# Kernel optimization log

Measured on AMD Instinct MI355X. Metric: run time of the kernel, lower is better.

Reference implementation:

```python
import jax, jax.numpy as jnp
import numpy as np

MSFA = 4
EPS = 1e-6

def _mosaic_channel_index(H, W, m):
    # channel selected at pixel (h, w) is (h % m) * m + (w % m)
    h = jnp.arange(H) % m
    w = jnp.arange(W) % m
    return (h[:, None] * m + w[None, :]).astype(jnp.int32)  # [H, W]

def get_msfa(x, m):
    # x: [B, C, H, W] with C == m*m. Equivalent to the one-hot mask-multiply-sum:
    # a per-pixel gather of the channel dictated by the mosaic pattern.
    B, C, H, W = x.shape
    ch = _mosaic_channel_index(H, W, m)  # [H, W]
    idx = jnp.broadcast_to(ch[None, None], (B, 1, H, W))
    return jnp.take_along_axis(x, idx, axis=1)[:, 0]  # [B, H, W]

def charbonnier_mean(a, b):
    d = a - b
    return jnp.mean(jnp.sqrt(d * d + EPS))

def setup_inputs() -> dict:
    key = jax.random.key(0)
    k1, k2 = jax.random.split(key)
    B, C, H, W = 8, MSFA * MSFA, 512, 512
    X = jax.random.normal(k1, (B, C, H, W), dtype=jnp.float32)
    Y = jax.random.normal(k2, (B, C, H, W), dtype=jnp.float32)
    return {"X": X, "Y": Y}

def reference(X, Y):
    return charbonnier_mean(get_msfa(X, MSFA), get_msfa(Y, MSFA))
```

## Files before the change

kernel.cpp:

```cpp
#include <hip/hip_runtime.h>


#define EPS_F 1e-6f

constexpr int kBlocks  = 1024;
constexpr int kThreads = 256;
constexpr int kNPix    = 8 * 512 * 512;
constexpr int kPerThr  = kNPix / (kBlocks * kThreads);

__global__ __launch_bounds__(kThreads) void msfa_charb_partial(
    const float* __restrict__ X, const float* __restrict__ Y,
    float* __restrict__ partial)
{
    const int tid      = blockIdx.x * kThreads + threadIdx.x;
    const int nthreads = kBlocks * kThreads;

    float acc = 0.0f;
#pragma unroll
    for (int it = 0; it < kPerThr; ++it) {
        const int idx = tid + it * nthreads;
        const int b   = idx >> 18;
        const int rem = idx & 0x3FFFF;
        const int h   = rem >> 9;
        const int w   = rem & 511;
        const int c   = ((h & 3) << 2) | (w & 3);
        const int off = (((b << 4) + c) << 18) + (h << 9) + w;
        const float d = X[off] - Y[off];
        acc += sqrtf(d * d + EPS_F);
    }

#pragma unroll
    for (int s = 32; s > 0; s >>= 1)
        acc += __shfl_down(acc, s, 64);

    __shared__ float sdata[kThreads / 64];
    const int lane = threadIdx.x & 63;
    const int wave = threadIdx.x >> 6;
    if (lane == 0) sdata[wave] = acc;
    __syncthreads();
    if (threadIdx.x == 0) {
        float t = 0.0f;
#pragma unroll
        for (int i = 0; i < kThreads / 64; ++i) t += sdata[i];
        partial[blockIdx.x] = t;
    }
}

__global__ __launch_bounds__(1024) void msfa_finalize(
    const float* __restrict__ partial, float* __restrict__ out)
{
    float v = partial[threadIdx.x];
#pragma unroll
    for (int s = 32; s > 0; s >>= 1)
        v += __shfl_down(v, s, 64);

    __shared__ float sdata[16];
    const int lane = threadIdx.x & 63;
    const int wave = threadIdx.x >> 6;
    if (lane == 0) sdata[wave] = v;
    __syncthreads();
    if (threadIdx.x == 0) {
        float t = 0.0f;
#pragma unroll
        for (int i = 0; i < 16; ++i) t += sdata[i];
        out[0] = t * (1.0f / (float)kNPix);
    }
}

extern "C" void kernel_launch(void* const* d_in, const int* in_sizes, int n_in,
                              void* d_out, int out_size, void* d_ws, size_t ws_size,
                              hipStream_t stream)
{
    const float* X = (const float*)d_in[0];
    const float* Y = (const float*)d_in[1];
    float* partial = (float*)d_ws;
    float* out     = (float*)d_out;

    msfa_charb_partial<<<kBlocks, kThreads, 0, stream>>>(X, Y, partial);
    msfa_finalize<<<1, 1024, 0, stream>>>(partial, out);
}
```

Baseline: 225.4 us.

## Remap threads to vectorized float4 loads grouped by mosaic column phase

Threads are remapped so that each wave shares one mosaic column phase and one channel plane. Each lane issues a contiguous float4 load and keeps the single component it needs, looping over the 8 batches. This replaces scattered scalar loads spread across four channel planes per wave with fully coalesced 16-byte accesses, cutting the number of memory transactions. Three quarters of each loaded vector is discarded, but DRAM sectors were already fetched whole in the old scheme.

```diff
diff --git a/kernel.cpp b/kernel.cpp
--- a/kernel.cpp
+++ b/kernel.cpp
@@ -6,26 +6,30 @@
 constexpr int kBlocks  = 1024;
 constexpr int kThreads = 256;
 constexpr int kNPix    = 8 * 512 * 512;
-constexpr int kPerThr  = kNPix / (kBlocks * kThreads);
+constexpr int kBatchF4 = 16 * 512 * 128;
 
 __global__ __launch_bounds__(kThreads) void msfa_charb_partial(
-    const float* __restrict__ X, const float* __restrict__ Y,
+    const float4* __restrict__ X4, const float4* __restrict__ Y4,
     float* __restrict__ partial)
 {
-    const int tid      = blockIdx.x * kThreads + threadIdx.x;
-    const int nthreads = kBlocks * kThreads;
+    const int tid = blockIdx.x * kThreads + threadIdx.x;
+    const int k = tid & 127;
+    const int r = (tid >> 7) & 127;
+    const int j = (tid >> 14) & 3;
+    const int g = tid >> 16;
+    const int h = (r << 2) | g;
+    const int c = (g << 2) | j;
+    const int base = (((c << 9) | h) << 7) | k;
 
     float acc = 0.0f;
 #pragma unroll
-    for (int it = 0; it < kPerThr; ++it) {
-        const int idx = tid + it * nthreads;
-        const int b   = idx >> 18;
-        const int rem = idx & 0x3FFFF;
-        const int h   = rem >> 9;
-        const int w   = rem & 511;
-        const int c   = ((h & 3) << 2) | (w & 3);
-        const int off = (((b << 4) + c) << 18) + (h << 9) + w;
-        const float d = X[off] - Y[off];
+    for (int b = 0; b < 8; ++b) {
+        const int f = base + b * kBatchF4;
+        const float4 x = X4[f];
+        const float4 y = Y4[f];
+        const float xv = (j == 0) ? x.x : (j == 1) ? x.y : (j == 2) ? x.z : x.w;
+        const float yv = (j == 0) ? y.x : (j == 1) ? y.y : (j == 2) ? y.z : y.w;
+        const float d = xv - yv;
         acc += sqrtf(d * d + EPS_F);
     }
 
@@ -71,11 +75,11 @@
                               void* d_out, int out_size, void* d_ws, size_t ws_size,
                               hipStream_t stream)
 {
-    const float* X = (const float*)d_in[0];
-    const float* Y = (const float*)d_in[1];
+    const float4* X4 = (const float4*)d_in[0];
+    const float4* Y4 = (const float4*)d_in[1];
     float* partial = (float*)d_ws;
     float* out     = (float*)d_out;
 
-    msfa_charb_partial<<<kBlocks, kThreads, 0, stream>>>(X, Y, partial);
+    msfa_charb_partial<<<kBlocks, kThreads, 0, stream>>>(X4, Y4, partial);
     msfa_finalize<<<1, 1024, 0, stream>>>(partial, out);
 }
```

Measured after the change: 226.7 us. No clear change (+0.6%).
